# Performance work log

Measured on AMD Instinct MI355X. Metric: run time of the kernel, lower is better.

Reference implementation:

```python
import jax, jax.numpy as jnp
import numpy as np

H = 1024      # hidden_size
I = 512       # moe_intermediate_size
E = 8         # n_routed_experts
K = 2         # num_experts_per_tok
SI = I * 2    # shared expert intermediate (n_shared_experts=2)
B, S = 2, 1024


def setup_inputs() -> dict:
    key = jax.random.key(0)
    ks = jax.random.split(key, 9)
    s = 0.02
    return {
        "x": jax.random.normal(ks[0], (B, S, H), jnp.float32),
        "gate_w": jax.random.normal(ks[1], (E, H), jnp.float32) * s,
        "lb_bias": jnp.zeros((E,), jnp.float32),
        "expert_gate_w": jax.random.normal(ks[2], (E, I, H), jnp.float32) * s,
        "expert_up_w": jax.random.normal(ks[3], (E, I, H), jnp.float32) * s,
        "expert_down_w": jax.random.normal(ks[4], (E, H, I), jnp.float32) * s,
        "shared_gate_w": jax.random.normal(ks[5], (SI, H), jnp.float32) * s,
        "shared_up_w": jax.random.normal(ks[6], (SI, H), jnp.float32) * s,
        "shared_down_w": jax.random.normal(ks[7], (H, SI), jnp.float32) * s,
    }


def _mlp(x, gw, uw, dw):
    # SwiGLU: down( silu(gate(x)) * up(x) )
    return (jax.nn.silu(x @ gw.T) * (x @ uw.T)) @ dw.T


def reference(x, gate_w, lb_bias, expert_gate_w, expert_up_w, expert_down_w,
              shared_gate_w, shared_up_w, shared_down_w):
    b, s, h = x.shape
    xf = x.reshape(-1, h)                                   # [T, H]
    # --- SimpleRouter (sigmoid scoring) ---
    logits = xf @ gate_w.T + lb_bias                        # [T, E]
    scores = jax.nn.sigmoid(logits.astype(jnp.float32))
    topw, topi = jax.lax.top_k(scores, K)                   # [T, K]
    topw = (topw / (topw.sum(-1, keepdims=True) + 1e-8)).astype(x.dtype)
    # --- _process_local: per-expert dispatch/compute/combine ---
    # Faithful to torch source: expert_weights[mask].mean(dim=-1) collapses to a
    # SCALAR per expert (mean routing weight over all tokens sent to that expert).
    out = jnp.zeros_like(xf)
    for e in range(E):
        m = (topi == e)                                     # [T, K]
        sel = m.any(axis=-1)                                # [T]
        cnt = m.sum()
        wmean = (topw * m).sum() / jnp.maximum(cnt, 1).astype(topw.dtype)
        y = _mlp(xf, expert_gate_w[e], expert_up_w[e], expert_down_w[e])  # [T, H]
        out = out + jnp.where(sel[:, None], y * wmean, jnp.zeros((), x.dtype))
    out = out.reshape(b, s, h)
    # --- shared experts ---
    out = out + _mlp(x, shared_gate_w, shared_up_w, shared_down_w)
    return out
```

## Files before the change

### kernel.cpp

```cpp
#include <hip/hip_runtime.h>

#define H_DIM 1024
#define I_DIM 512
#define NE 8
#define SI_DIM 1024
#define NT 2048

typedef __bf16 bf16;
typedef __bf16 bf16x4 __attribute__((ext_vector_type(4)));
typedef __bf16 bf16x8 __attribute__((ext_vector_type(8)));
typedef float f32x4 __attribute__((ext_vector_type(4)));

#define W_GU 0ull
#define W_DN 8388608ull
#define W_SGU 12582912ull
#define W_SDN 14680064ull
#define W_TOT 15728640ull

#define NWB 15360
#define NRB 512

#define OFF_CNT 0
#define OFF_WM 64
#define OFF_TOPI 1024
#define OFF_TOPW (OFF_TOPI + NT * 8)
#define OFF_LISTS (OFF_TOPW + NT * 8)
#define OFF_WB (OFF_LISTS + NE * NT * 4)
#define OFF_XB (OFF_WB + (size_t)W_TOT * 2)
#define OFF_ACTE (OFF_XB + (size_t)NT * H_DIM * 2)
#define OFF_ACTS (OFF_ACTE + (size_t)NE * NT * I_DIM * 2)

__device__ __forceinline__ bf16x4 cvt4(f32x4 v) {
  bf16x4 r;
  r.x = (bf16)v.x; r.y = (bf16)v.y; r.z = (bf16)v.z; r.w = (bf16)v.w;
  return r;
}

__device__ __forceinline__ void glds16(const bf16* g, bf16* l) {
  __builtin_amdgcn_global_load_lds(
      (const __attribute__((address_space(1))) unsigned int*)g,
      (__attribute__((address_space(3))) unsigned int*)l, 16, 0, 0);
}

__global__ __launch_bounds__(256) void prep_kernel(
    const float* __restrict__ x, const float* __restrict__ gw,
    const float* __restrict__ lb, const float* __restrict__ eg,
    const float* __restrict__ eu, const float* __restrict__ ed,
    const float* __restrict__ sg, const float* __restrict__ su,
    const float* __restrict__ sd, bf16* __restrict__ wb,
    bf16* __restrict__ xb, int2* __restrict__ topi,
    float2* __restrict__ topw) {
  const int bx = blockIdx.x;
  const int tid = threadIdx.x;
  if (bx < NWB) {
    size_t i = ((size_t)bx * 256 + tid) * 4;
    const float* src;
    if (i < W_DN) {
      size_t z = i >> 20;
      int rem = (int)(i & ((1u << 20) - 1));
      int rp = rem >> 10, k = rem & 1023;
      int b = rp >> 4;
      int sr = ((b >> 1) << 4) | (rp & 15);
      src = ((b & 1) ? eu : eg) + (z << 19) + ((size_t)sr << 10) + k;
    } else if (i < W_SGU) {
      src = ed + (i - W_DN);
    } else if (i < W_SDN) {
      int rem = (int)(i - W_SGU);
      int rp = rem >> 10, k = rem & 1023;
      int b = rp >> 4;
      int sr = ((b >> 1) << 4) | (rp & 15);
      src = ((b & 1) ? su : sg) + ((size_t)sr << 10) + k;
    } else {
      src = sd + (i - W_SDN);
    }
    *(bf16x4*)(wb + i) = cvt4(*(const f32x4*)src);
  } else {
    const int lane = tid & 63;
    const int t = (bx - NWB) * 4 + (tid >> 6);
    const float* xr = x + (size_t)t * H_DIM;
    bf16* xw = xb + (size_t)t * H_DIM;
    float s[NE];
#pragma unroll
    for (int e = 0; e < NE; e++) s[e] = 0.f;
#pragma unroll
    for (int k0 = 0; k0 < H_DIM; k0 += 256) {
      f32x4 xv = *(const f32x4*)(xr + k0 + lane * 4);
      *(bf16x4*)(xw + k0 + lane * 4) = cvt4(xv);
#pragma unroll
      for (int e = 0; e < NE; e++) {
        f32x4 gv = *(const f32x4*)(gw + e * H_DIM + k0 + lane * 4);
        s[e] += xv.x * gv.x + xv.y * gv.y + xv.z * gv.z + xv.w * gv.w;
      }
    }
#pragma unroll
    for (int e = 0; e < NE; e++) {
      float v = s[e];
#pragma unroll
      for (int off = 32; off > 0; off >>= 1) v += __shfl_xor(v, off);
      s[e] = v;
    }
    if (lane == 0) {
      float sc[NE];
#pragma unroll
      for (int e = 0; e < NE; e++) sc[e] = 1.f / (1.f + expf(-(s[e] + lb[e])));
      int i1 = 0;
#pragma unroll
      for (int e = 1; e < NE; e++)
        if (sc[e] > sc[i1]) i1 = e;
      int i2 = -1;
#pragma unroll
      for (int e = 0; e < NE; e++) {
        if (e == i1) continue;
        if (i2 < 0 || sc[e] > sc[i2]) i2 = e;
      }
      float w1 = sc[i1], w2 = sc[i2];
      float inv = 1.f / (w1 + w2 + 1e-8f);
      topi[t] = make_int2(i1, i2);
      topw[t] = make_float2(w1 * inv, w2 * inv);
    }
  }
}

__global__ __launch_bounds__(256) void build_kernel(
    const int2* __restrict__ topi, const float2* __restrict__ topw,
    int* __restrict__ cnt, float* __restrict__ wm, int* __restrict__ lists) {
  const int e = blockIdx.x;
  const int wave = threadIdx.x >> 6, lane = threadIdx.x & 63;
  __shared__ int wc[4];
  __shared__ float wf[4];
  const int tbeg = wave * (NT / 4), tend = tbeg + NT / 4;

  int c = 0;
  float wa = 0.f;
  for (int t0 = tbeg; t0 < tend; t0 += 64) {
    int2 ti = topi[t0 + lane];
    float2 tw = topw[t0 + lane];
    bool hit = (ti.x == e) || (ti.y == e);
    float w = (ti.x == e) ? tw.x : ((ti.y == e) ? tw.y : 0.f);
    c += __popcll(__ballot(hit));
#pragma unroll
    for (int off = 32; off > 0; off >>= 1) w += __shfl_xor(w, off);
    wa += w;
  }
  if (lane == 0) { wc[wave] = c; wf[wave] = wa; }
  __syncthreads();
  int pos = 0;
  for (int w = 0; w < wave; w++) pos += wc[w];
  for (int t0 = tbeg; t0 < tend; t0 += 64) {
    int t = t0 + lane;
    int2 ti = topi[t];
    bool hit = (ti.x == e) || (ti.y == e);
    unsigned long long m = __ballot(hit);
    int pre = __popcll(m & ((1ull << lane) - 1ull));
    if (hit) lists[e * NT + pos + pre] = t;
    pos += __popcll(m);
  }
  if (threadIdx.x == 0) {
    int ctot = wc[0] + wc[1] + wc[2] + wc[3];
    cnt[e] = ctot;
    wm[e] = (wf[0] + wf[1] + wf[2] + wf[3]) / (float)(ctot > 0 ? ctot : 1);
  }
}

__global__ __launch_bounds__(256, 4) void gemm_gu(
    const bf16* __restrict__ wb, const bf16* __restrict__ xb,
    const int* __restrict__ cnt, const int* __restrict__ lists,
    bf16* __restrict__ act_e, bf16* __restrict__ act_s) {
  const int b = blockIdx.x;
  int z, ct, rt;
  if (b < 2048) {
    z = b & 7;
    int q = b >> 3;
    ct = q & 7;
    rt = q >> 3;
  } else {
    z = NE;
    int s = b - 2048;
    int u = s >> 3;
    ct = (s & 7) * 2 + (u & 1);
    rt = u >> 1;
  }
  const int tid = threadIdx.x;
  __shared__ int rows_s[64];
  __shared__ __align__(16) bf16 As[64 * 64];
  __shared__ __align__(16) bf16 Bs[128 * 64];
  int mrem, ldc;
  bf16* Cb;
  const bf16* Bb;
  if (z < NE) {
    int c = cnt[z];
    if (rt * 64 >= c) return;
    mrem = c - rt * 64;
    if (tid < 64)
      rows_s[tid] = lists[z * NT + rt * 64 + (tid < mrem ? tid : mrem - 1)];
    Bb = wb + W_GU + ((size_t)z << 20) + (size_t)ct * 128 * H_DIM;
    Cb = act_e + ((size_t)z * NT + rt * 64) * I_DIM;
    ldc = I_DIM;
  } else {
    mrem = 64;
    if (tid < 64) rows_s[tid] = rt * 64 + tid;
    Bb = wb + W_SGU + (size_t)ct * 128 * H_DIM;
    Cb = act_s + (size_t)rt * 64 * SI_DIM;
    ldc = SI_DIM;
  }
  __syncthreads();

  const int lane = tid & 63, wave = tid >> 6;
  const int mw = (wave & 1) * 32, nw = (wave >> 1) * 64;
  const int l15 = lane & 15, quad = lane >> 4;
  const int srow = tid >> 3;
  const int cch = tid & 7;
  const int p8 = cch * 8;
  const int sx = (l15 & 7) * 8;

  const bf16 *ap[2], *bp[4];
  int alo[2], blo[4];
#pragma unroll
  for (int r = 0; r < 2; r++) {
    int R = srow + r * 32;
    int gs = (cch ^ (R & 7)) * 8;
    ap[r] = xb + (size_t)rows_s[R] * H_DIM + gs;
    alo[r] = R * 64 + p8;
  }
#pragma unroll
  for (int r = 0; r < 4; r++) {
    int R = srow + r * 32;
    int gs = (cch ^ (R & 7)) * 8;
    bp[r] = Bb + (size_t)R * H_DIM + gs;
    blo[r] = R * 64 + p8;
  }

  f32x4 acc[2][4] = {};
  for (int k0 = 0; k0 < H_DIM; k0 += 64) {
#pragma unroll
    for (int r = 0; r < 2; r++) glds16(ap[r] + k0, &As[alo[r]]);
#pragma unroll
    for (int r = 0; r < 4; r++) glds16(bp[r] + k0, &Bs[blo[r]]);
    __syncthreads();
#pragma unroll
    for (int kk = 0; kk < 2; kk++) {
      const int ko = (kk * 4 + quad) * 8;
      bf16x8 av[2], bv[4];
#pragma unroll
      for (int i = 0; i < 2; i++)
        av[i] = *(const bf16x8*)&As[(mw + i * 16 + l15) * 64 + (ko ^ sx)];
#pragma unroll
      for (int j = 0; j < 4; j++)
        bv[j] = *(const bf16x8*)&Bs[(nw + j * 16 + l15) * 64 + (ko ^ sx)];
#pragma unroll
      for (int i = 0; i < 2; i++)
#pragma unroll
        for (int j = 0; j < 4; j++)
          acc[i][j] = __builtin_amdgcn_mfma_f32_16x16x32_bf16(av[i], bv[j], acc[i][j], 0, 0, 0);
    }
    __syncthreads();
  }

#pragma unroll
  for (int i = 0; i < 2; i++) {
#pragma unroll
    for (int rg = 0; rg < 4; rg++) {
      int rl = mw + i * 16 + quad * 4 + rg;
      if (rl < mrem) {
#pragma unroll
        for (int jp = 0; jp < 2; jp++) {
          float g = acc[i][jp * 2][rg];
          float u = acc[i][jp * 2 + 1][rg];
          int c = ct * 64 + (nw >> 1) + jp * 16 + l15;
          Cb[(size_t)rl * ldc + c] = (bf16)((g / (1.f + __expf(-g))) * u);
        }
      }
    }
  }
}

__global__ __launch_bounds__(256, 4) void gemm_down(
    const bf16* __restrict__ wb, const bf16* __restrict__ act_e,
    const bf16* __restrict__ act_s, const int* __restrict__ cnt,
    const float* __restrict__ wm, const int* __restrict__ lists,
    float* __restrict__ out) {
  const int b = blockIdx.x;
  int z, ct, rt;
  if (b < 2048) {
    z = b & 7;
    int q = b >> 3;
    ct = q & 7;
    rt = q >> 3;
  } else {
    z = NE;
    int s = b - 2048;
    ct = s & 7;
    rt = s >> 3;
  }
  const int tid = threadIdx.x;
  __shared__ int rows_s[64];
  __shared__ __align__(16) bf16 As[64 * 64];
  __shared__ __align__(16) bf16 Bs[128 * 64];
  int K, mrem;
  const bf16 *Ab, *Bb;
  if (z < NE) {
    int c = cnt[z];
    if (rt * 64 >= c) return;
    mrem = c - rt * 64;
    if (tid < 64)
      rows_s[tid] = lists[z * NT + rt * 64 + (tid < mrem ? tid : mrem - 1)];
    Ab = act_e + ((size_t)z * NT + rt * 64) * I_DIM;
    K = I_DIM;
    Bb = wb + W_DN + ((size_t)z << 19) + (size_t)ct * 128 * I_DIM;
  } else {
    mrem = 64;
    if (tid < 64) rows_s[tid] = rt * 64 + tid;
    Ab = act_s + (size_t)rt * 64 * SI_DIM;
    K = SI_DIM;
    Bb = wb + W_SDN + (size_t)ct * 128 * SI_DIM;
  }
  __syncthreads();

  const int lane = tid & 63, wave = tid >> 6;
  const int mw = (wave & 1) * 32, nw = (wave >> 1) * 64;
  const int l15 = lane & 15, quad = lane >> 4;
  const int srow = tid >> 3;
  const int cch = tid & 7;
  const int p8 = cch * 8;
  const int sx = (l15 & 7) * 8;

  const bf16 *ap[2], *bp[4];
  int alo[2], blo[4];
#pragma unroll
  for (int r = 0; r < 2; r++) {
    int R = srow + r * 32;
    int gs = (cch ^ (R & 7)) * 8;
    ap[r] = Ab + (size_t)R * K + gs;
    alo[r] = R * 64 + p8;
  }
#pragma unroll
  for (int r = 0; r < 4; r++) {
    int R = srow + r * 32;
    int gs = (cch ^ (R & 7)) * 8;
    bp[r] = Bb + (size_t)R * K + gs;
    blo[r] = R * 64 + p8;
  }

  f32x4 acc[2][4] = {};
  for (int k0 = 0; k0 < K; k0 += 64) {
#pragma unroll
    for (int r = 0; r < 2; r++) glds16(ap[r] + k0, &As[alo[r]]);
#pragma unroll
    for (int r = 0; r < 4; r++) glds16(bp[r] + k0, &Bs[blo[r]]);
    __syncthreads();
#pragma unroll
    for (int kk = 0; kk < 2; kk++) {
      const int ko = (kk * 4 + quad) * 8;
      bf16x8 av[2], bv[4];
#pragma unroll
      for (int i = 0; i < 2; i++)
        av[i] = *(const bf16x8*)&As[(mw + i * 16 + l15) * 64 + (ko ^ sx)];
#pragma unroll
      for (int j = 0; j < 4; j++)
        bv[j] = *(const bf16x8*)&Bs[(nw + j * 16 + l15) * 64 + (ko ^ sx)];
#pragma unroll
      for (int i = 0; i < 2; i++)
#pragma unroll
        for (int j = 0; j < 4; j++)
          acc[i][j] = __builtin_amdgcn_mfma_f32_16x16x32_bf16(av[i], bv[j], acc[i][j], 0, 0, 0);
    }
    __syncthreads();
  }

  const float wsc = (z < NE) ? wm[z] : 1.f;
#pragma unroll
  for (int i = 0; i < 2; i++) {
#pragma unroll
    for (int rg = 0; rg < 4; rg++) {
      int rl = mw + i * 16 + quad * 4 + rg;
      if (rl < mrem) {
        int t = rows_s[rl];
        float* orow = out + (size_t)t * H_DIM + ct * 128 + nw;
#pragma unroll
        for (int j = 0; j < 4; j++)
          atomicAdd(&orow[j * 16 + l15], wsc * acc[i][j][rg]);
      }
    }
  }
}

extern "C" void kernel_launch(void* const* d_in, const int* in_sizes, int n_in,
                              void* d_out, int out_size, void* d_ws,
                              size_t ws_size, hipStream_t stream) {
  (void)in_sizes; (void)n_in; (void)out_size; (void)ws_size;
  const float* x  = (const float*)d_in[0];
  const float* gw = (const float*)d_in[1];
  const float* lb = (const float*)d_in[2];
  const float* eg = (const float*)d_in[3];
  const float* eu = (const float*)d_in[4];
  const float* ed = (const float*)d_in[5];
  const float* sg = (const float*)d_in[6];
  const float* su = (const float*)d_in[7];
  const float* sd = (const float*)d_in[8];
  float* out = (float*)d_out;
  char* ws = (char*)d_ws;

  int* cnt     = (int*)(ws + OFF_CNT);
  float* wm    = (float*)(ws + OFF_WM);
  int2* topi   = (int2*)(ws + OFF_TOPI);
  float2* topw = (float2*)(ws + OFF_TOPW);
  int* lists   = (int*)(ws + OFF_LISTS);
  bf16* wb     = (bf16*)(ws + OFF_WB);
  bf16* xb     = (bf16*)(ws + OFF_XB);
  bf16* act_e  = (bf16*)(ws + OFF_ACTE);
  bf16* act_s  = (bf16*)(ws + OFF_ACTS);

  hipMemsetAsync(d_out, 0, (size_t)NT * H_DIM * sizeof(float), stream);
  prep_kernel<<<NWB + NRB, 256, 0, stream>>>(x, gw, lb, eg, eu, ed, sg, su, sd,
                                             wb, xb, topi, topw);
  build_kernel<<<NE, 256, 0, stream>>>(topi, topw, cnt, wm, lists);
  gemm_gu<<<2560, 256, 0, stream>>>(wb, xb, cnt, lists, act_e, act_s);
  gemm_down<<<2304, 256, 0, stream>>>(wb, act_e, act_s, cnt, wm, lists, out);
}
```

Baseline: 201.4 us.

## Fuse fp32-to-bf16 weight conversion into GEMM tile loads and fold output zeroing

Removes the separate pass that converted all expert and shared weights to a bf16 workspace. The GEMMs now read fp32 weights directly, convert them in registers and store them into swizzled LDS, replacing async global-to-LDS loads for the B operand. The output memset is folded into the prep kernel as extra zeroing blocks. The aim is to drop a full read-write pass over about 60MB of weights and one launch. The cost is reading weights as fp32 inside the GEMMs, repeated across row tiles, with the loads going through registers. Launch bounds also drop from 4 to 2 blocks per SM.

```diff
diff --git a/kernel.cpp b/kernel.cpp
--- a/kernel.cpp
+++ b/kernel.cpp
@@ -11,22 +11,15 @@
 typedef __bf16 bf16x8 __attribute__((ext_vector_type(8)));
 typedef float f32x4 __attribute__((ext_vector_type(4)));
 
-#define W_GU 0ull
-#define W_DN 8388608ull
-#define W_SGU 12582912ull
-#define W_SDN 14680064ull
-#define W_TOT 15728640ull
-
-#define NWB 15360
 #define NRB 512
+#define NZB 2048
 
 #define OFF_CNT 0
 #define OFF_WM 64
 #define OFF_TOPI 1024
 #define OFF_TOPW (OFF_TOPI + NT * 8)
 #define OFF_LISTS (OFF_TOPW + NT * 8)
-#define OFF_WB (OFF_LISTS + NE * NT * 4)
-#define OFF_XB (OFF_WB + (size_t)W_TOT * 2)
+#define OFF_XB (OFF_LISTS + NE * NT * 4)
 #define OFF_ACTE (OFF_XB + (size_t)NT * H_DIM * 2)
 #define OFF_ACTS (OFF_ACTE + (size_t)NE * NT * I_DIM * 2)
 
@@ -44,39 +37,14 @@
 
 __global__ __launch_bounds__(256) void prep_kernel(
     const float* __restrict__ x, const float* __restrict__ gw,
-    const float* __restrict__ lb, const float* __restrict__ eg,
-    const float* __restrict__ eu, const float* __restrict__ ed,
-    const float* __restrict__ sg, const float* __restrict__ su,
-    const float* __restrict__ sd, bf16* __restrict__ wb,
-    bf16* __restrict__ xb, int2* __restrict__ topi,
-    float2* __restrict__ topw) {
+    const float* __restrict__ lb, bf16* __restrict__ xb,
+    int2* __restrict__ topi, float2* __restrict__ topw,
+    float* __restrict__ out) {
   const int bx = blockIdx.x;
   const int tid = threadIdx.x;
-  if (bx < NWB) {
-    size_t i = ((size_t)bx * 256 + tid) * 4;
-    const float* src;
-    if (i < W_DN) {
-      size_t z = i >> 20;
-      int rem = (int)(i & ((1u << 20) - 1));
-      int rp = rem >> 10, k = rem & 1023;
-      int b = rp >> 4;
-      int sr = ((b >> 1) << 4) | (rp & 15);
-      src = ((b & 1) ? eu : eg) + (z << 19) + ((size_t)sr << 10) + k;
-    } else if (i < W_SGU) {
-      src = ed + (i - W_DN);
-    } else if (i < W_SDN) {
-      int rem = (int)(i - W_SGU);
-      int rp = rem >> 10, k = rem & 1023;
-      int b = rp >> 4;
-      int sr = ((b >> 1) << 4) | (rp & 15);
-      src = ((b & 1) ? su : sg) + ((size_t)sr << 10) + k;
-    } else {
-      src = sd + (i - W_SDN);
-    }
-    *(bf16x4*)(wb + i) = cvt4(*(const f32x4*)src);
-  } else {
+  if (bx < NRB) {
     const int lane = tid & 63;
-    const int t = (bx - NWB) * 4 + (tid >> 6);
+    const int t = bx * 4 + (tid >> 6);
     const float* xr = x + (size_t)t * H_DIM;
     bf16* xw = xb + (size_t)t * H_DIM;
     float s[NE];
@@ -118,6 +86,10 @@
       topi[t] = make_int2(i1, i2);
       topw[t] = make_float2(w1 * inv, w2 * inv);
     }
+  } else {
+    size_t j = ((size_t)(bx - NRB) * 256 + tid) * 4;
+    f32x4 zz = {0.f, 0.f, 0.f, 0.f};
+    *(f32x4*)(out + j) = zz;
   }
 }
 
@@ -162,10 +134,12 @@
   }
 }
 
-__global__ __launch_bounds__(256, 4) void gemm_gu(
-    const bf16* __restrict__ wb, const bf16* __restrict__ xb,
-    const int* __restrict__ cnt, const int* __restrict__ lists,
-    bf16* __restrict__ act_e, bf16* __restrict__ act_s) {
+__global__ __launch_bounds__(256, 2) void gemm_gu(
+    const float* __restrict__ eg, const float* __restrict__ eu,
+    const float* __restrict__ sg, const float* __restrict__ su,
+    const bf16* __restrict__ xb, const int* __restrict__ cnt,
+    const int* __restrict__ lists, bf16* __restrict__ act_e,
+    bf16* __restrict__ act_s) {
   const int b = blockIdx.x;
   int z, ct, rt;
   if (b < 2048) {
@@ -184,22 +158,26 @@
   __shared__ int rows_s[64];
   __shared__ __align__(16) bf16 As[64 * 64];
   __shared__ __align__(16) bf16 Bs[128 * 64];
+  const int t15 = tid & 15;
+  const int trow = tid >> 4;
   int mrem, ldc;
   bf16* Cb;
-  const bf16* Bb;
+  const float *be, *bo;
   if (z < NE) {
     int c = cnt[z];
     if (rt * 64 >= c) return;
     mrem = c - rt * 64;
     if (tid < 64)
       rows_s[tid] = lists[z * NT + rt * 64 + (tid < mrem ? tid : mrem - 1)];
-    Bb = wb + W_GU + ((size_t)z << 20) + (size_t)ct * 128 * H_DIM;
+    be = eg + ((size_t)z << 19) + t15 * 4;
+    bo = eu + ((size_t)z << 19) + t15 * 4;
     Cb = act_e + ((size_t)z * NT + rt * 64) * I_DIM;
     ldc = I_DIM;
   } else {
     mrem = 64;
     if (tid < 64) rows_s[tid] = rt * 64 + tid;
-    Bb = wb + W_SGU + (size_t)ct * 128 * H_DIM;
+    be = sg + t15 * 4;
+    bo = su + t15 * 4;
     Cb = act_s + (size_t)rt * 64 * SI_DIM;
     ldc = SI_DIM;
   }
@@ -213,8 +191,8 @@
   const int p8 = cch * 8;
   const int sx = (l15 & 7) * 8;
 
-  const bf16 *ap[2], *bp[4];
-  int alo[2], blo[4];
+  const bf16* ap[2];
+  int alo[2];
 #pragma unroll
   for (int r = 0; r < 2; r++) {
     int R = srow + r * 32;
@@ -222,20 +200,23 @@
     ap[r] = xb + (size_t)rows_s[R] * H_DIM + gs;
     alo[r] = R * 64 + p8;
   }
-#pragma unroll
-  for (int r = 0; r < 4; r++) {
-    int R = srow + r * 32;
-    int gs = (cch ^ (R & 7)) * 8;
-    bp[r] = Bb + (size_t)R * H_DIM + gs;
-    blo[r] = R * 64 + p8;
-  }
+  int ro[4];
+#pragma unroll
+  for (int j = 0; j < 4; j++) ro[j] = (((ct * 4 + j) << 4) + trow) << 10;
+  const int bofs = trow * 128 + (((t15 >> 1) ^ (trow & 7)) * 16) + (tid & 1) * 8;
+  char* BsB = (char*)Bs;
 
   f32x4 acc[2][4] = {};
   for (int k0 = 0; k0 < H_DIM; k0 += 64) {
 #pragma unroll
     for (int r = 0; r < 2; r++) glds16(ap[r] + k0, &As[alo[r]]);
 #pragma unroll
-    for (int r = 0; r < 4; r++) glds16(bp[r] + k0, &Bs[blo[r]]);
+    for (int j = 0; j < 4; j++) {
+      f32x4 wg = *(const f32x4*)(be + ro[j] + k0);
+      f32x4 wu = *(const f32x4*)(bo + ro[j] + k0);
+      *(bf16x4*)(BsB + bofs + (2 * j) * 2048) = cvt4(wg);
+      *(bf16x4*)(BsB + bofs + (2 * j + 1) * 2048) = cvt4(wu);
+    }
     __syncthreads();
 #pragma unroll
     for (int kk = 0; kk < 2; kk++) {
@@ -274,11 +255,11 @@
   }
 }
 
-__global__ __launch_bounds__(256, 4) void gemm_down(
-    const bf16* __restrict__ wb, const bf16* __restrict__ act_e,
-    const bf16* __restrict__ act_s, const int* __restrict__ cnt,
-    const float* __restrict__ wm, const int* __restrict__ lists,
-    float* __restrict__ out) {
+__global__ __launch_bounds__(256, 2) void gemm_down(
+    const float* __restrict__ ed, const float* __restrict__ sd,
+    const bf16* __restrict__ act_e, const bf16* __restrict__ act_s,
+    const int* __restrict__ cnt, const float* __restrict__ wm,
+    const int* __restrict__ lists, float* __restrict__ out) {
   const int b = blockIdx.x;
   int z, ct, rt;
   if (b < 2048) {
@@ -296,8 +277,11 @@
   __shared__ int rows_s[64];
   __shared__ __align__(16) bf16 As[64 * 64];
   __shared__ __align__(16) bf16 Bs[128 * 64];
+  const int t15 = tid & 15;
+  const int trow = tid >> 4;
   int K, mrem;
-  const bf16 *Ab, *Bb;
+  const bf16* Ab;
+  const float* bd;
   if (z < NE) {
     int c = cnt[z];
     if (rt * 64 >= c) return;
@@ -306,13 +290,13 @@
       rows_s[tid] = lists[z * NT + rt * 64 + (tid < mrem ? tid : mrem - 1)];
     Ab = act_e + ((size_t)z * NT + rt * 64) * I_DIM;
     K = I_DIM;
-    Bb = wb + W_DN + ((size_t)z << 19) + (size_t)ct * 128 * I_DIM;
+    bd = ed + (size_t)z * (H_DIM * I_DIM) + t15 * 4;
   } else {
     mrem = 64;
     if (tid < 64) rows_s[tid] = rt * 64 + tid;
     Ab = act_s + (size_t)rt * 64 * SI_DIM;
     K = SI_DIM;
-    Bb = wb + W_SDN + (size_t)ct * 128 * SI_DIM;
+    bd = sd + t15 * 4;
   }
   __syncthreads();
 
@@ -324,8 +308,8 @@
   const int p8 = cch * 8;
   const int sx = (l15 & 7) * 8;
 
-  const bf16 *ap[2], *bp[4];
-  int alo[2], blo[4];
+  const bf16* ap[2];
+  int alo[2];
 #pragma unroll
   for (int r = 0; r < 2; r++) {
     int R = srow + r * 32;
@@ -333,20 +317,21 @@
     ap[r] = Ab + (size_t)R * K + gs;
     alo[r] = R * 64 + p8;
   }
-#pragma unroll
-  for (int r = 0; r < 4; r++) {
-    int R = srow + r * 32;
-    int gs = (cch ^ (R & 7)) * 8;
-    bp[r] = Bb + (size_t)R * K + gs;
-    blo[r] = R * 64 + p8;
-  }
+  int ro[8];
+#pragma unroll
+  for (int i = 0; i < 8; i++) ro[i] = (ct * 128 + trow + 16 * i) * K;
+  const int bofs = trow * 128 + (((t15 >> 1) ^ (trow & 7)) * 16) + (tid & 1) * 8;
+  char* BsB = (char*)Bs;
 
   f32x4 acc[2][4] = {};
   for (int k0 = 0; k0 < K; k0 += 64) {
 #pragma unroll
     for (int r = 0; r < 2; r++) glds16(ap[r] + k0, &As[alo[r]]);
 #pragma unroll
-    for (int r = 0; r < 4; r++) glds16(bp[r] + k0, &Bs[blo[r]]);
+    for (int i = 0; i < 8; i++) {
+      f32x4 w = *(const f32x4*)(bd + ro[i] + k0);
+      *(bf16x4*)(BsB + bofs + i * 2048) = cvt4(w);
+    }
     __syncthreads();
 #pragma unroll
     for (int kk = 0; kk < 2; kk++) {
@@ -405,15 +390,14 @@
   int2* topi   = (int2*)(ws + OFF_TOPI);
   float2* topw = (float2*)(ws + OFF_TOPW);
   int* lists   = (int*)(ws + OFF_LISTS);
-  bf16* wb     = (bf16*)(ws + OFF_WB);
   bf16* xb     = (bf16*)(ws + OFF_XB);
   bf16* act_e  = (bf16*)(ws + OFF_ACTE);
   bf16* act_s  = (bf16*)(ws + OFF_ACTS);
 
-  hipMemsetAsync(d_out, 0, (size_t)NT * H_DIM * sizeof(float), stream);
-  prep_kernel<<<NWB + NRB, 256, 0, stream>>>(x, gw, lb, eg, eu, ed, sg, su, sd,
-                                             wb, xb, topi, topw);
+  prep_kernel<<<NRB + NZB, 256, 0, stream>>>(x, gw, lb, xb, topi, topw, out);
   build_kernel<<<NE, 256, 0, stream>>>(topi, topw, cnt, wm, lists);
-  gemm_gu<<<2560, 256, 0, stream>>>(wb, xb, cnt, lists, act_e, act_s);
-  gemm_down<<<2304, 256, 0, stream>>>(wb, act_e, act_s, cnt, wm, lists, out);
-}
+  gemm_gu<<<2560, 256, 0, stream>>>(eg, eu, sg, su, xb, cnt, lists, act_e,
+                                    act_s);
+  gemm_down<<<2304, 256, 0, stream>>>(ed, sd, act_e, act_s, cnt, wm, lists,
+                                      out);
+}
```

Result: slower. 245.0 us (+21.6%).

## Fuse expert list building and output zeroing into prep kernel via atomics

Applied to the files above, without the earlier changes.

Removes the separate build_kernel by having the router lane atomically append tokens to per-expert lists and accumulate per-expert weight sums inside prep_kernel. Output zeroing also moves into extra prep blocks instead of a full-size memset, leaving only a small memset of the counters. The mean weight is now computed in gemm_down from the sum and the count. This saves a launch and a serial tiny-grid kernel, but list order becomes nondeterministic and the atomic float sum order changes.

```diff
diff --git a/kernel.cpp b/kernel.cpp
--- a/kernel.cpp
+++ b/kernel.cpp
@@ -19,12 +19,11 @@
 
 #define NWB 15360
 #define NRB 512
+#define NZB 2048
 
 #define OFF_CNT 0
-#define OFF_WM 64
-#define OFF_TOPI 1024
-#define OFF_TOPW (OFF_TOPI + NT * 8)
-#define OFF_LISTS (OFF_TOPW + NT * 8)
+#define OFF_WS 64
+#define OFF_LISTS 1024
 #define OFF_WB (OFF_LISTS + NE * NT * 4)
 #define OFF_XB (OFF_WB + (size_t)W_TOT * 2)
 #define OFF_ACTE (OFF_XB + (size_t)NT * H_DIM * 2)
@@ -48,8 +47,8 @@
     const float* __restrict__ eu, const float* __restrict__ ed,
     const float* __restrict__ sg, const float* __restrict__ su,
     const float* __restrict__ sd, bf16* __restrict__ wb,
-    bf16* __restrict__ xb, int2* __restrict__ topi,
-    float2* __restrict__ topw) {
+    bf16* __restrict__ xb, int* __restrict__ cnt, float* __restrict__ wsum,
+    int* __restrict__ lists, float* __restrict__ out) {
   const int bx = blockIdx.x;
   const int tid = threadIdx.x;
   if (bx < NWB) {
@@ -74,7 +73,7 @@
       src = sd + (i - W_SDN);
     }
     *(bf16x4*)(wb + i) = cvt4(*(const f32x4*)src);
-  } else {
+  } else if (bx < NWB + NRB) {
     const int lane = tid & 63;
     const int t = (bx - NWB) * 4 + (tid >> 6);
     const float* xr = x + (size_t)t * H_DIM;
@@ -115,50 +114,17 @@
       }
       float w1 = sc[i1], w2 = sc[i2];
       float inv = 1.f / (w1 + w2 + 1e-8f);
-      topi[t] = make_int2(i1, i2);
-      topw[t] = make_float2(w1 * inv, w2 * inv);
-    }
-  }
-}
-
-__global__ __launch_bounds__(256) void build_kernel(
-    const int2* __restrict__ topi, const float2* __restrict__ topw,
-    int* __restrict__ cnt, float* __restrict__ wm, int* __restrict__ lists) {
-  const int e = blockIdx.x;
-  const int wave = threadIdx.x >> 6, lane = threadIdx.x & 63;
-  __shared__ int wc[4];
-  __shared__ float wf[4];
-  const int tbeg = wave * (NT / 4), tend = tbeg + NT / 4;
-
-  int c = 0;
-  float wa = 0.f;
-  for (int t0 = tbeg; t0 < tend; t0 += 64) {
-    int2 ti = topi[t0 + lane];
-    float2 tw = topw[t0 + lane];
-    bool hit = (ti.x == e) || (ti.y == e);
-    float w = (ti.x == e) ? tw.x : ((ti.y == e) ? tw.y : 0.f);
-    c += __popcll(__ballot(hit));
-#pragma unroll
-    for (int off = 32; off > 0; off >>= 1) w += __shfl_xor(w, off);
-    wa += w;
-  }
-  if (lane == 0) { wc[wave] = c; wf[wave] = wa; }
-  __syncthreads();
-  int pos = 0;
-  for (int w = 0; w < wave; w++) pos += wc[w];
-  for (int t0 = tbeg; t0 < tend; t0 += 64) {
-    int t = t0 + lane;
-    int2 ti = topi[t];
-    bool hit = (ti.x == e) || (ti.y == e);
-    unsigned long long m = __ballot(hit);
-    int pre = __popcll(m & ((1ull << lane) - 1ull));
-    if (hit) lists[e * NT + pos + pre] = t;
-    pos += __popcll(m);
-  }
-  if (threadIdx.x == 0) {
-    int ctot = wc[0] + wc[1] + wc[2] + wc[3];
-    cnt[e] = ctot;
-    wm[e] = (wf[0] + wf[1] + wf[2] + wf[3]) / (float)(ctot > 0 ? ctot : 1);
+      int p1 = atomicAdd(&cnt[i1], 1);
+      lists[i1 * NT + p1] = t;
+      atomicAdd(&wsum[i1], w1 * inv);
+      int p2 = atomicAdd(&cnt[i2], 1);
+      lists[i2 * NT + p2] = t;
+      atomicAdd(&wsum[i2], w2 * inv);
+    }
+  } else {
+    size_t j = ((size_t)(bx - NWB - NRB) * 256 + tid) * 4;
+    f32x4 zz = {0.f, 0.f, 0.f, 0.f};
+    *(f32x4*)(out + j) = zz;
   }
 }
 
@@ -277,7 +243,7 @@
 __global__ __launch_bounds__(256, 4) void gemm_down(
     const bf16* __restrict__ wb, const bf16* __restrict__ act_e,
     const bf16* __restrict__ act_s, const int* __restrict__ cnt,
-    const float* __restrict__ wm, const int* __restrict__ lists,
+    const float* __restrict__ wsum, const int* __restrict__ lists,
     float* __restrict__ out) {
   const int b = blockIdx.x;
   int z, ct, rt;
@@ -297,11 +263,13 @@
   __shared__ __align__(16) bf16 As[64 * 64];
   __shared__ __align__(16) bf16 Bs[128 * 64];
   int K, mrem;
+  float wsc;
   const bf16 *Ab, *Bb;
   if (z < NE) {
     int c = cnt[z];
     if (rt * 64 >= c) return;
     mrem = c - rt * 64;
+    wsc = wsum[z] / (float)(c > 0 ? c : 1);
     if (tid < 64)
       rows_s[tid] = lists[z * NT + rt * 64 + (tid < mrem ? tid : mrem - 1)];
     Ab = act_e + ((size_t)z * NT + rt * 64) * I_DIM;
@@ -309,6 +277,7 @@
     Bb = wb + W_DN + ((size_t)z << 19) + (size_t)ct * 128 * I_DIM;
   } else {
     mrem = 64;
+    wsc = 1.f;
     if (tid < 64) rows_s[tid] = rt * 64 + tid;
     Ab = act_s + (size_t)rt * 64 * SI_DIM;
     K = SI_DIM;
@@ -367,7 +336,6 @@
     __syncthreads();
   }
 
-  const float wsc = (z < NE) ? wm[z] : 1.f;
 #pragma unroll
   for (int i = 0; i < 2; i++) {
 #pragma unroll
@@ -401,19 +369,17 @@
   char* ws = (char*)d_ws;
 
   int* cnt     = (int*)(ws + OFF_CNT);
-  float* wm    = (float*)(ws + OFF_WM);
-  int2* topi   = (int2*)(ws + OFF_TOPI);
-  float2* topw = (float2*)(ws + OFF_TOPW);
+  float* wsum  = (float*)(ws + OFF_WS);
   int* lists   = (int*)(ws + OFF_LISTS);
   bf16* wb     = (bf16*)(ws + OFF_WB);
   bf16* xb     = (bf16*)(ws + OFF_XB);
   bf16* act_e  = (bf16*)(ws + OFF_ACTE);
   bf16* act_s  = (bf16*)(ws + OFF_ACTS);
 
-  hipMemsetAsync(d_out, 0, (size_t)NT * H_DIM * sizeof(float), stream);
-  prep_kernel<<<NWB + NRB, 256, 0, stream>>>(x, gw, lb, eg, eu, ed, sg, su, sd,
-                                             wb, xb, topi, topw);
-  build_kernel<<<NE, 256, 0, stream>>>(topi, topw, cnt, wm, lists);
+  hipMemsetAsync(ws, 0, 128, stream);
+  prep_kernel<<<NWB + NRB + NZB, 256, 0, stream>>>(x, gw, lb, eg, eu, ed, sg,
+                                                   su, sd, wb, xb, cnt, wsum,
+                                                   lists, out);
   gemm_gu<<<2560, 256, 0, stream>>>(wb, xb, cnt, lists, act_e, act_s);
-  gemm_down<<<2304, 256, 0, stream>>>(wb, act_e, act_s, cnt, wm, lists, out);
-}
+  gemm_down<<<2304, 256, 0, stream>>>(wb, act_e, act_s, cnt, wsum, lists, out);
+}
```

Measured after the change: 260.0 us. 1.29x slower.
